# Performance work log

Hardware: AMD Instinct MI355X
Metric: run time of the kernel (lower is better)

Reference implementation:

```python
import jax, jax.numpy as jnp
import numpy as np

B, N, E, H = 2, 4096, 1024, 16
HD = E // H                      # head_dim = 64
R = 8                            # LoRA rank
LORA_SCALE = 16.0 / R            # alpha / r = 2.0
BUCKET_SIZES = (256, 64, 16)


def setup_inputs() -> dict:
    key = jax.random.key(0)
    ks = jax.random.split(key, 24)
    inp = {"x": jax.random.normal(ks[0], (B, N, E), jnp.float32)}
    inp["wb_coarse"] = jax.random.randint(ks[1], (B, N), 0, 16)
    inp["wb_mid"] = jax.random.randint(ks[2], (B, N), 0, 64)
    inp["wb_fine"] = jax.random.randint(ks[3], (B, N), 0, 256)
    i = 4
    for name in ("q", "k", "v", "o"):
        inp[f"W{name}"] = jax.random.normal(ks[i], (E, E), jnp.float32) / np.sqrt(E); i += 1
        inp[f"b{name}"] = jax.random.normal(ks[i], (E,), jnp.float32) * 0.01; i += 1
        inp[f"A{name}"] = jax.random.normal(ks[i], (R, E), jnp.float32) / np.sqrt(E); i += 1
        inp[f"B{name}"] = jax.random.normal(ks[i], (E, R), jnp.float32) * 0.01; i += 1
    return inp


def _lora(x, W, b, A, Bm):
    # F.linear(x, W, b) + scale * x @ A.T @ B.T   (dropout=0 in eval)
    return x @ W.T + b + LORA_SCALE * ((x @ A.T) @ Bm.T)


def _chunked_attn(q, k, v, bidx, C):
    # q,k,v: [BH, N, D]; bidx: [BH, N] int; C: chunk size (divides N)
    BH, Nn, D = q.shape
    sidx = jnp.argsort(bidx, axis=1)
    uidx = jnp.argsort(sidx, axis=1)
    g = lambda t, i: jnp.take_along_axis(t, i[..., None], axis=1)
    qs, ks_, vs = g(q, sidx), g(k, sidx), g(v, sidx)
    nc = Nn // C
    qs = qs.reshape(BH, nc, C, D)
    ks_ = ks_.reshape(BH, nc, C, D)
    vs = vs.reshape(BH, nc, C, D)
    # previous chunk (look-back of one chunk); chunk 0 has no previous -> masked
    k_prev = jnp.concatenate([jnp.zeros_like(ks_[:, :1]), ks_[:, :-1]], axis=1)
    v_prev = jnp.concatenate([jnp.zeros_like(vs[:, :1]), vs[:, :-1]], axis=1)
    k_cat = jnp.concatenate([k_prev, ks_], axis=2)   # [BH, nc, 2C, D]
    v_cat = jnp.concatenate([v_prev, vs], axis=2)
    scores = jnp.einsum('bncd,bnkd->bnck', qs, k_cat) / jnp.sqrt(jnp.asarray(D, qs.dtype))
    # mask look-back keys for chunk 0 (torch path attends only within chunk 0)
    chunk_ids = jnp.arange(nc)[:, None, None]        # [nc,1,1]
    key_pos = jnp.arange(2 * C)[None, None, :]       # [1,1,2C]
    neg = jnp.finfo(scores.dtype).min
    scores = jnp.where((chunk_ids == 0) & (key_pos < C), neg, scores)
    attn = jax.nn.softmax(scores, axis=-1)
    out = jnp.einsum('bnck,bnkd->bncd', attn, v_cat).reshape(BH, Nn, D)
    return jnp.take_along_axis(out, uidx[..., None], axis=1)


def reference(x, wb_coarse, wb_mid, wb_fine,
              Wq, bq, Aq, Bq, Wk, bk, Ak, Bk,
              Wv, bv, Av, Bv, Wo, bo, Ao, Bo):
    q = _lora(x, Wq, bq, Aq, Bq)
    k = _lora(x, Wk, bk, Ak, Bk)
    v = _lora(x, Wv, bv, Av, Bv)
    to_heads = lambda t: t.reshape(B, N, H, HD).transpose(0, 2, 1, 3).reshape(B * H, N, HD)
    qh, kh, vh = to_heads(q), to_heads(k), to_heads(v)
    expand = lambda w: jnp.broadcast_to(w[:, None, :], (B, H, N)).reshape(B * H, N)
    wbs = (expand(wb_coarse), expand(wb_mid), expand(wb_fine))
    outs = (_chunked_attn(qh, kh, vh, wbs[0], BUCKET_SIZES[0])
            + _chunked_attn(qh, kh, vh, wbs[1], BUCKET_SIZES[1])
            + _chunked_attn(qh, kh, vh, wbs[2], BUCKET_SIZES[2])) / 3.0
    outs = outs.reshape(B, H, N, HD).transpose(0, 2, 1, 3).reshape(B, N, E)
    return _lora(outs, Wo, bo, Ao, Bo)
```

## Files before the change

kernel.cpp:

```cpp
#include <hip/hip_runtime.h>
#include <cstdint>
#include <cstddef>

#define BDIM 2
#define NTOK 4096
#define EDIM 1024
#define HEADS 16
#define HDIM 64
#define MROWS (BDIM * NTOK)

typedef unsigned short u16;
typedef __attribute__((ext_vector_type(8))) short bf16x8;
typedef __attribute__((ext_vector_type(8))) unsigned short u16x8;
typedef __attribute__((ext_vector_type(4))) float f32x4;

#define MFMA(a, b, c) __builtin_amdgcn_mfma_f32_16x16x32_bf16(a, b, c, 0, 0, 0)
#define BAR() asm volatile("s_barrier" ::: "memory")
#define SETPRIO(p) __builtin_amdgcn_s_setprio(p)

__device__ inline void split2(float x, u16& h, u16& l) {
    union { float f; unsigned u; } a;
    a.f = x;
    unsigned uh = a.u + 0x7fff + ((a.u >> 16) & 1);
    h = (u16)(uh >> 16);
    union { unsigned u; float f; } hf; hf.u = (unsigned)h << 16;
    a.f = x - hf.f;
    unsigned ul = a.u + 0x7fff + ((a.u >> 16) & 1);
    l = (u16)(ul >> 16);
}

__device__ inline u16 bf16rne(float x) {
    union { float f; unsigned u; } a; a.f = x;
    unsigned r = a.u + 0x7fff + ((a.u >> 16) & 1);
    return (u16)(r >> 16);
}

#define GLL(gp, lp) __builtin_amdgcn_global_load_lds( \
    (const __attribute__((address_space(1))) unsigned*)(gp), \
    (__attribute__((address_space(3))) unsigned*)(lp), 16, 0, 0)

__global__ __launch_bounds__(256) void build_weff4_kernel(
    const float* __restrict__ W0, const float* __restrict__ A0, const float* __restrict__ B0,
    const float* __restrict__ W1, const float* __restrict__ A1, const float* __restrict__ B1,
    const float* __restrict__ W2, const float* __restrict__ A2, const float* __restrict__ B2,
    const float* __restrict__ W3, const float* __restrict__ A3, const float* __restrict__ B3,
    u16* __restrict__ dh0, u16* __restrict__ dl0,
    u16* __restrict__ dh1, u16* __restrict__ dl1,
    u16* __restrict__ dh2, u16* __restrict__ dl2,
    u16* __restrict__ dh3, u16* __restrict__ dl3)
{
    int s = blockIdx.y;
    const float* W = (s == 0) ? W0 : (s == 1) ? W1 : (s == 2) ? W2 : W3;
    const float* A = (s == 0) ? A0 : (s == 1) ? A1 : (s == 2) ? A2 : A3;
    const float* Bm = (s == 0) ? B0 : (s == 1) ? B1 : (s == 2) ? B2 : B3;
    u16* dh = (s == 0) ? dh0 : (s == 1) ? dh1 : (s == 2) ? dh2 : dh3;
    u16* dl = (s == 0) ? dl0 : (s == 1) ? dl1 : (s == 2) ? dl2 : dl3;

    int idx = blockIdx.x * 256 + threadIdx.x;
    int o = idx >> 10, i = idx & 1023;
    float sum = 0.f;
#pragma unroll
    for (int r = 0; r < 8; ++r) sum += Bm[o * 8 + r] * A[r * 1024 + i];
    float w = W[idx] + 2.0f * sum;
    u16 h, l;
    split2(w, h, l);
    dh[idx] = h; dl[idx] = l;
}

__global__ __launch_bounds__(256) void split_kernel(
    const float* __restrict__ src, u16* __restrict__ dh, u16* __restrict__ dl)
{
    int idx = blockIdx.x * 256 + threadIdx.x;
    float4 v = ((const float4*)src)[idx];
    ushort4 h, l;
    split2(v.x, h.x, l.x);
    split2(v.y, h.y, l.y);
    split2(v.z, h.z, l.z);
    split2(v.w, h.w, l.w);
    ((ushort4*)dh)[idx] = h;
    ((ushort4*)dl)[idx] = l;
}

__global__ __launch_bounds__(256) void sort3_kernel(
    const int* __restrict__ w0, const int* __restrict__ w1,
    const int* __restrict__ w2, int* __restrict__ sidx)
{
    __shared__ int sb[NTOK];
    __shared__ int cnt[32][256];
    __shared__ int gb[256];
    const int* srcs[3] = {w0, w1, w2};
    int t = threadIdx.x;
    const int* w = srcs[blockIdx.y] + blockIdx.x * NTOK;
    int* outp = sidx + ((int)blockIdx.y * BDIM + (int)blockIdx.x) * NTOK;

    for (int i = t; i < NTOK; i += 256) sb[i] = w[i];
    for (int i = t; i < 32 * 256; i += 256) ((int*)cnt)[i] = 0;
    __syncthreads();

    int g = t >> 3;
#pragma unroll
    for (int e = 0; e < 16; ++e)
        atomicAdd(&cnt[g][sb[g * 128 + (t & 7) + 8 * e]], 1);
    __syncthreads();

    int run = 0;
#pragma unroll
    for (int gg = 0; gg < 32; ++gg) {
        int c = cnt[gg][t];
        cnt[gg][t] = run;
        run += c;
    }
    gb[t] = run;
    __syncthreads();
    if (t == 0) {
        int acc = 0;
        for (int v = 0; v < 256; ++v) { int c = gb[v]; gb[v] = acc; acc += c; }
    }
    __syncthreads();
    for (int i = t; i < 32 * 256; i += 256) {
        int v = i & 255, gg = i >> 8;
        cnt[gg][v] += gb[v];
    }
    __syncthreads();

    if (t < 32) {
        int base = t * 128;
        for (int e = 0; e < 128; ++e) {
            int v = sb[base + e];
            int p = cnt[t][v]++;
            outp[p] = base + e;
        }
    }
}

__global__ __launch_bounds__(512, 2) void gemm_qk_kernel(
    const u16* __restrict__ Xh, const u16* __restrict__ Xl,
    const u16* __restrict__ Wh, const u16* __restrict__ Wl,
    const float* __restrict__ bq, const float* __restrict__ bk,
    u16* __restrict__ qh, u16* __restrict__ ql,
    u16* __restrict__ kh, u16* __restrict__ kl)
{
    __shared__ __align__(16) unsigned char smem[147456];
    u16* lds = (u16*)smem;
    const int PA_h = 0, PA_l = 8192, PB_h = 16384, PB_l = 20480;

    int t = threadIdx.x;
    int lane = t & 63, wave = t >> 6;
    int bid = blockIdx.x;
    int wg = (bid & 7) * 64 + (bid >> 3);
    int bx = wg & 15, by = wg >> 4;
    int m0 = by * 256, n0 = bx * 128;

    int lrow = lane & 15, lq = lane >> 4;
    size_t aoff = (size_t)(m0 + wave * 32 + lrow) * EDIM + lq * 8;
    size_t boff = (size_t)(n0 + wave * 16 + lrow) * EDIM + lq * 8;
    int slabA = wave * 2;
    int sA0 = (wave >> 1) * 4;
    int sB0 = (wave & 1) * 4;
    f32x4 acc[4][4] = {};

#pragma unroll
    for (int tt = 0; tt < 2; ++tt) {
        u16* sbuf = lds + tt * 24576;
        int kk = tt * 32;
        GLL(Xh + aoff + kk,             sbuf + PA_h + (slabA + 0) * 512);
        GLL(Xh + aoff + kk + 16 * EDIM, sbuf + PA_h + (slabA + 1) * 512);
        GLL(Xl + aoff + kk,             sbuf + PA_l + (slabA + 0) * 512);
        GLL(Xl + aoff + kk + 16 * EDIM, sbuf + PA_l + (slabA + 1) * 512);
        GLL(Wh + boff + kk, sbuf + PB_h + wave * 512);
        GLL(Wl + boff + kk, sbuf + PB_l + wave * 512);
    }
    asm volatile("s_waitcnt vmcnt(6)" ::: "memory");
    BAR();

    for (int t32 = 0; t32 < 32; ++t32) {
        u16* rb = lds + (t32 % 3) * 24576;
        u16* sbuf = lds + ((t32 + 2) % 3) * 24576;
        bool pf = (t32 + 2) < 32;
        int kn = (t32 + 2) * 32;
        bf16x8 bhf[4], blf[4];
#pragma unroll
        for (int p = 0; p < 4; ++p) {
            if (p == 0) {
#pragma unroll
                for (int j = 0; j < 4; ++j) {
                    bhf[j] = *(const bf16x8*)(rb + PB_h + (sB0 + j) * 512 + lane * 8);
                    blf[j] = *(const bf16x8*)(rb + PB_l + (sB0 + j) * 512 + lane * 8);
                }
            }
            bf16x8 aph = *(const bf16x8*)(rb + PA_h + (sA0 + p) * 512 + lane * 8);
            bf16x8 apl = *(const bf16x8*)(rb + PA_l + (sA0 + p) * 512 + lane * 8);
            if (pf) {
                if (p == 0) {
                    GLL(Xh + aoff + kn,             sbuf + PA_h + (slabA + 0) * 512);
                    GLL(Xh + aoff + kn + 16 * EDIM, sbuf + PA_h + (slabA + 1) * 512);
                } else if (p == 1) {
                    GLL(Xl + aoff + kn,             sbuf + PA_l + (slabA + 0) * 512);
                    GLL(Xl + aoff + kn + 16 * EDIM, sbuf + PA_l + (slabA + 1) * 512);
                } else if (p == 2) {
                    GLL(Wh + boff + kn, sbuf + PB_h + wave * 512);
                    GLL(Wl + boff + kn, sbuf + PB_l + wave * 512);
                }
            }
            BAR();
            SETPRIO(1);
#pragma unroll
            for (int j = 0; j < 4; ++j) {
                acc[p][j] = MFMA(aph, bhf[j], acc[p][j]);
                acc[p][j] = MFMA(aph, blf[j], acc[p][j]);
                acc[p][j] = MFMA(apl, bhf[j], acc[p][j]);
            }
            SETPRIO(0);
            if (p == 3) {
                if (pf) asm volatile("s_waitcnt vmcnt(6)" ::: "memory");
                else    asm volatile("s_waitcnt vmcnt(0)" ::: "memory");
            }
            BAR();
        }
    }

    int proj = n0 >> 10;
    const float* bias = proj ? bk : bq;
    u16* ohp = proj ? kh : qh;
    u16* olp = proj ? kl : ql;
    int wm = (wave >> 1) * 64, wn = (wave & 1) * 64;
    int q4 = lane >> 4, l16 = lane & 15;
    int cb = (n0 & 1023) + wn;
    float bj[4];
#pragma unroll
    for (int j = 0; j < 4; ++j) bj[j] = bias[cb + j * 16 + l16];
    float* repw = (float*)smem + wave * 2176;
    int r8 = lane >> 3, c8 = lane & 7;
#pragma unroll
    for (int gph = 0; gph < 2; ++gph) {
#pragma unroll
        for (int ii = 0; ii < 2; ++ii)
#pragma unroll
            for (int j = 0; j < 4; ++j)
#pragma unroll
                for (int r = 0; r < 4; ++r)
                    repw[(ii * 16 + q4 * 4 + r) * 68 + j * 16 + l16] =
                        acc[gph * 2 + ii][j][r] + bj[j];
#pragma unroll
        for (int rg = 0; rg < 4; ++rg) {
            int lr = rg * 8 + r8;
            float4 f0 = *(float4*)(repw + lr * 68 + c8 * 8);
            float4 f1 = *(float4*)(repw + lr * 68 + c8 * 8 + 4);
            float fa[8] = {f0.x, f0.y, f0.z, f0.w, f1.x, f1.y, f1.z, f1.w};
            size_t off = (size_t)(m0 + wm + gph * 32 + lr) * EDIM + cb + c8 * 8;
            u16x8 hv, lv;
#pragma unroll
            for (int e = 0; e < 8; ++e) {
                float v = fa[e];
                if (proj == 0) v *= 0.125f;
                u16 hh, ll;
                split2(v, hh, ll);
                hv[e] = hh; lv[e] = ll;
            }
            *(u16x8*)(ohp + off) = hv;
            *(u16x8*)(olp + off) = lv;
        }
    }
}

__global__ __launch_bounds__(512, 2) void gemm_v_kernel(
    const u16* __restrict__ Xh, const u16* __restrict__ Wv,
    const float* __restrict__ bv, u16* __restrict__ vh)
{
    __shared__ __align__(16) unsigned char smem[73728];
    u16* lds = (u16*)smem;

    int t = threadIdx.x;
    int lane = t & 63, wave = t >> 6;
    int bid = blockIdx.x;
    int wg = (bid & 7) * 32 + (bid >> 3);
    int bx = wg & 7, by = wg >> 3;
    int m0 = by * 256, nc0 = bx * 128;

    int lrow = lane & 15, lq = lane >> 4;
    size_t aoff = (size_t)(m0 + wave * 32 + lrow) * EDIM + lq * 8;
    size_t boff = (size_t)(nc0 + wave * 16 + lrow) * EDIM + lq * 8;
    int slabA = wave * 2;
    int sA0 = (wave >> 1) * 4;
    int sB0 = (wave & 1) * 4;
    f32x4 acc[4][4] = {};

#pragma unroll
    for (int tt = 0; tt < 2; ++tt) {
        u16* sbuf = lds + tt * 12288;
        int kk = tt * 32;
        GLL(Xh + aoff + kk,             sbuf + (slabA + 0) * 512);
        GLL(Xh + aoff + kk + 16 * EDIM, sbuf + (slabA + 1) * 512);
        GLL(Wv + boff + kk,             sbuf + 8192 + wave * 512);
    }
    asm volatile("s_waitcnt vmcnt(3)" ::: "memory");
    BAR();

    for (int t32 = 0; t32 < 32; ++t32) {
        u16* rb = lds + (t32 % 3) * 12288;
        u16* sbuf = lds + ((t32 + 2) % 3) * 12288;
        bool pf = (t32 + 2) < 32;
        int kn = (t32 + 2) * 32;

        bf16x8 bhf[4];
#pragma unroll
        for (int j = 0; j < 4; ++j)
            bhf[j] = *(const bf16x8*)(rb + 8192 + (sB0 + j) * 512 + lane * 8);
        bf16x8 a0 = *(const bf16x8*)(rb + (sA0 + 0) * 512 + lane * 8);
        bf16x8 a1 = *(const bf16x8*)(rb + (sA0 + 1) * 512 + lane * 8);
        if (pf) {
            GLL(Xh + aoff + kn,             sbuf + (slabA + 0) * 512);
            GLL(Xh + aoff + kn + 16 * EDIM, sbuf + (slabA + 1) * 512);
        }
        BAR();
        SETPRIO(1);
#pragma unroll
        for (int j = 0; j < 4; ++j) {
            acc[0][j] = MFMA(a0, bhf[j], acc[0][j]);
            acc[1][j] = MFMA(a1, bhf[j], acc[1][j]);
        }
        SETPRIO(0);
        BAR();

        bf16x8 a2 = *(const bf16x8*)(rb + (sA0 + 2) * 512 + lane * 8);
        bf16x8 a3 = *(const bf16x8*)(rb + (sA0 + 3) * 512 + lane * 8);
        if (pf) GLL(Wv + boff + kn, sbuf + 8192 + wave * 512);
        BAR();
        SETPRIO(1);
#pragma unroll
        for (int j = 0; j < 4; ++j) {
            acc[2][j] = MFMA(a2, bhf[j], acc[2][j]);
            acc[3][j] = MFMA(a3, bhf[j], acc[3][j]);
        }
        SETPRIO(0);
        if (pf) asm volatile("s_waitcnt vmcnt(3)" ::: "memory");
        else    asm volatile("s_waitcnt vmcnt(0)" ::: "memory");
        BAR();
    }

    int wm = (wave >> 1) * 64, wn = (wave & 1) * 64;
    int q4 = lane >> 4, l16 = lane & 15;
    int cb = nc0 + wn;
    float bj[4];
#pragma unroll
    for (int j = 0; j < 4; ++j) bj[j] = bv[cb + j * 16 + l16];
    float* repw = (float*)smem + wave * 2176;
    int r8 = lane >> 3, c8 = lane & 7;
#pragma unroll
    for (int gph = 0; gph < 2; ++gph) {
#pragma unroll
        for (int ii = 0; ii < 2; ++ii)
#pragma unroll
            for (int j = 0; j < 4; ++j)
#pragma unroll
                for (int r = 0; r < 4; ++r)
                    repw[(ii * 16 + q4 * 4 + r) * 68 + j * 16 + l16] =
                        acc[gph * 2 + ii][j][r] + bj[j];
#pragma unroll
        for (int rg = 0; rg < 4; ++rg) {
            int lr = rg * 8 + r8;
            float4 f0 = *(float4*)(repw + lr * 68 + c8 * 8);
            float4 f1 = *(float4*)(repw + lr * 68 + c8 * 8 + 4);
            float fa[8] = {f0.x, f0.y, f0.z, f0.w, f1.x, f1.y, f1.z, f1.w};
            size_t off = (size_t)(m0 + wm + gph * 32 + lr) * EDIM + cb + c8 * 8;
            u16x8 hv;
#pragma unroll
            for (int e = 0; e < 8; ++e) hv[e] = bf16rne(fa[e]);
            *(u16x8*)(vh + off) = hv;
        }
    }
}

__global__ __launch_bounds__(512, 2) void gemm_o_kernel(
    const u16* __restrict__ Xh, const u16* __restrict__ Xl,
    const u16* __restrict__ Wh, const u16* __restrict__ Wl,
    const float* __restrict__ bias, float* __restrict__ Y)
{
    __shared__ __align__(16) unsigned char smem[147456];
    u16* lds = (u16*)smem;
    const int PA_h = 0, PA_l = 8192, PB_h = 16384, PB_l = 20480;

    int t = threadIdx.x;
    int lane = t & 63, wave = t >> 6;
    int bid = blockIdx.x;
    int wg = (bid & 7) * 32 + (bid >> 3);
    int bx = wg & 7, by = wg >> 3;
    int m0 = by * 256, n0 = bx * 128;

    int lrow = lane & 15, lq = lane >> 4;
    size_t aoff = (size_t)(m0 + wave * 32 + lrow) * EDIM + lq * 8;
    size_t boff = (size_t)(n0 + wave * 16 + lrow) * EDIM + lq * 8;
    int slabA = wave * 2;
    int sA0 = (wave >> 1) * 4;
    int sB0 = (wave & 1) * 4;
    f32x4 acc[4][4] = {};

#pragma unroll
    for (int tt = 0; tt < 2; ++tt) {
        u16* sbuf = lds + tt * 24576;
        int kk = tt * 32;
        GLL(Xh + aoff + kk,             sbuf + PA_h + (slabA + 0) * 512);
        GLL(Xh + aoff + kk + 16 * EDIM, sbuf + PA_h + (slabA + 1) * 512);
        GLL(Xl + aoff + kk,             sbuf + PA_l + (slabA + 0) * 512);
        GLL(Xl + aoff + kk + 16 * EDIM, sbuf + PA_l + (slabA + 1) * 512);
        GLL(Wh + boff + kk, sbuf + PB_h + wave * 512);
        GLL(Wl + boff + kk, sbuf + PB_l + wave * 512);
    }
    asm volatile("s_waitcnt vmcnt(6)" ::: "memory");
    BAR();

    for (int t32 = 0; t32 < 32; ++t32) {
        u16* rb = lds + (t32 % 3) * 24576;
        u16* sbuf = lds + ((t32 + 2) % 3) * 24576;
        bool pf = (t32 + 2) < 32;
        int kn = (t32 + 2) * 32;
        bf16x8 bhf[4], blf[4];
#pragma unroll
        for (int p = 0; p < 4; ++p) {
            if (p == 0) {
#pragma unroll
                for (int j = 0; j < 4; ++j) {
                    bhf[j] = *(const bf16x8*)(rb + PB_h + (sB0 + j) * 512 + lane * 8);
                    blf[j] = *(const bf16x8*)(rb + PB_l + (sB0 + j) * 512 + lane * 8);
                }
            }
            bf16x8 aph = *(const bf16x8*)(rb + PA_h + (sA0 + p) * 512 + lane * 8);
            bf16x8 apl = *(const bf16x8*)(rb + PA_l + (sA0 + p) * 512 + lane * 8);
            if (pf) {
                if (p == 0) {
                    GLL(Xh + aoff + kn,             sbuf + PA_h + (slabA + 0) * 512);
                    GLL(Xh + aoff + kn + 16 * EDIM, sbuf + PA_h + (slabA + 1) * 512);
                } else if (p == 1) {
                    GLL(Xl + aoff + kn,             sbuf + PA_l + (slabA + 0) * 512);
                    GLL(Xl + aoff + kn + 16 * EDIM, sbuf + PA_l + (slabA + 1) * 512);
                } else if (p == 2) {
                    GLL(Wh + boff + kn, sbuf + PB_h + wave * 512);
                    GLL(Wl + boff + kn, sbuf + PB_l + wave * 512);
                }
            }
            BAR();
            SETPRIO(1);
#pragma unroll
            for (int j = 0; j < 4; ++j) {
                acc[p][j] = MFMA(aph, bhf[j], acc[p][j]);
                acc[p][j] = MFMA(aph, blf[j], acc[p][j]);
                acc[p][j] = MFMA(apl, bhf[j], acc[p][j]);
            }
            SETPRIO(0);
            if (p == 3) {
                if (pf) asm volatile("s_waitcnt vmcnt(6)" ::: "memory");
                else    asm volatile("s_waitcnt vmcnt(0)" ::: "memory");
            }
            BAR();
        }
    }

    int wm = (wave >> 1) * 64, wn = (wave & 1) * 64;
    int col_in = lane & 15, rquad = lane >> 4;
#pragma unroll
    for (int j = 0; j < 4; ++j) {
        int col = n0 + wn + j * 16 + col_in;
        float bvv = bias[col];
#pragma unroll
        for (int i = 0; i < 4; ++i) {
            int mbase = m0 + wm + i * 16 + rquad * 4;
#pragma unroll
            for (int r = 0; r < 4; ++r)
                Y[(size_t)(mbase + r) * EDIM + col] = acc[i][j][r] + bvv;
        }
    }
}

template <int C, bool ACC, bool OSPLIT>
__global__ __launch_bounds__(256, 3) void attn_mfma_kernel(
    const u16* __restrict__ Qh, const u16* __restrict__ Ql,
    const u16* __restrict__ Kh, const u16* __restrict__ Kl,
    const u16* __restrict__ Vh, const int* __restrict__ sidx,
    float* __restrict__ out, u16* __restrict__ osh, u16* __restrict__ osl)
{
    __shared__ u16 KfH[2][4096], KfL[2][4096];
    __shared__ u16 VL[64 * 72];
    __shared__ u16 PbH[4 * 16 * 56];

    int t = threadIdx.x;
    int lane = t & 63, wave = t >> 6;
    int quad = lane >> 4, l16 = lane & 15;
    int bh = blockIdx.y, b = bh >> 4, h = bh & 15;
    int p0 = blockIdx.x * 128;
    const int* sxb = sidx + b * NTOK;

    int ptile[2], ws_[2], we_[2];
    bf16x8 qhf[2][2], qlf[2][2];
#pragma unroll
    for (int tq = 0; tq < 2; ++tq) {
        ptile[tq] = p0 + wave * 32 + tq * 16;
        int c = ptile[tq] / C;
        ws_[tq] = (c > 0) ? (c - 1) * C : 0;
        we_[tq] = (c + 1) * C;
        int qrow = sxb[ptile[tq] + l16];
        size_t rb = (size_t)(b * NTOK + qrow) * EDIM + h * HDIM + quad * 8;
#pragma unroll
        for (int kk = 0; kk < 2; ++kk) {
            qhf[tq][kk] = *(const bf16x8*)(Qh + rb + kk * 32);
            qlf[tq][kk] = *(const bf16x8*)(Ql + rb + kk * 32);
        }
    }

    f32x4 oacc[2][4] = {};
    float lpart[2][4] = {};
    float mrun[2] = {-1e30f, -1e30f};

    int c0 = p0 / C, c1 = (p0 + 127) / C;
    int kmin = (c0 > 0) ? (c0 - 1) * C : 0;
    int kmax = (c1 + 1) * C;
    int nsteps = (kmax - kmin + 63) >> 6;

    {
        int tok = sxb[min(kmin + wave * 16 + l16, NTOK - 1)];
        size_t rb = (size_t)(b * NTOK + tok) * EDIM + h * HDIM + quad * 8;
        GLL(Kh + rb,      &KfH[0][(wave * 2 + 0) * 512]);
        GLL(Kh + rb + 32, &KfH[0][(wave * 2 + 1) * 512]);
        GLL(Kl + rb,      &KfL[0][(wave * 2 + 0) * 512]);
        GLL(Kl + rb + 32, &KfL[0][(wave * 2 + 1) * 512]);
        bf16x8 vreg[2];
#pragma unroll
        for (int it = 0; it < 2; ++it) {
            int c = it * 256 + t;
            int key = c & 63, dg = c >> 6;
            int tok2 = sxb[min(kmin + key, NTOK - 1)];
            vreg[it] = *(const bf16x8*)(Vh + (size_t)(b * NTOK + tok2) * EDIM + h * HDIM + dg * 8);
        }
#pragma unroll
        for (int it = 0; it < 2; ++it) {
            int c = it * 256 + t;
            int key = c & 63, dg = c >> 6;
#pragma unroll
            for (int e = 0; e < 8; ++e)
                VL[(dg * 8 + e) * 72 + key] = (u16)vreg[it][e];
        }
        asm volatile("s_waitcnt vmcnt(0)" ::: "memory");
        __syncthreads();
    }

    int pb = 0;
    for (int s = 0; s < nsteps; ++s) {
        int ks = kmin + s * 64;
        int nk = min(64, kmax - ks);
        bool pf = (s + 1) < nsteps;
        bf16x8 vreg[2];
        if (pf) {
            int ks2 = ks + 64;
            int tok = sxb[min(ks2 + wave * 16 + l16, NTOK - 1)];
            size_t rb = (size_t)(b * NTOK + tok) * EDIM + h * HDIM + quad * 8;
            GLL(Kh + rb,      &KfH[pb ^ 1][(wave * 2 + 0) * 512]);
            GLL(Kh + rb + 32, &KfH[pb ^ 1][(wave * 2 + 1) * 512]);
            GLL(Kl + rb,      &KfL[pb ^ 1][(wave * 2 + 0) * 512]);
            GLL(Kl + rb + 32, &KfL[pb ^ 1][(wave * 2 + 1) * 512]);
#pragma unroll
            for (int it = 0; it < 2; ++it) {
                int c = it * 256 + t;
                int key = c & 63, dg = c >> 6;
                int tok2 = sxb[min(ks2 + key, NTOK - 1)];
                vreg[it] = *(const bf16x8*)(Vh + (size_t)(b * NTOK + tok2) * EDIM + h * HDIM + dg * 8);
            }
        }

        int jlo0 = max(ks, ws_[0]) - ks, jhi0 = min(ks + nk, we_[0]) - ks;
        int jlo1 = max(ks, ws_[1]) - ks, jhi1 = min(ks + nk, we_[1]) - ks;
        bool e0 = jlo0 < jhi0, e1 = jlo1 < jhi1;
        if (e0 || e1) {
            int glo = e0 ? (e1 ? min(jlo0, jlo1) : jlo0) : jlo1;
            int ghi = e0 ? (e1 ? max(jhi0, jhi1) : jhi0) : jhi1;
            const u16* kfh = &KfH[pb][0];
            const u16* kfl = &KfL[pb][0];

            for (int g0 = glo & ~31; g0 < ghi; g0 += 32) {
                int s0i = g0 >> 4;
                int s1i = min(s0i + 1, 3);
                bf16x8 kh0[2], kl0[2], kh1[2], kl1[2];
#pragma unroll
                for (int kk = 0; kk < 2; ++kk) {
                    kh0[kk] = *(const bf16x8*)(kfh + ((s0i * 2 + kk) * 64 + lane) * 8);
                    kl0[kk] = *(const bf16x8*)(kfl + ((s0i * 2 + kk) * 64 + lane) * 8);
                    kh1[kk] = *(const bf16x8*)(kfh + ((s1i * 2 + kk) * 64 + lane) * 8);
                    kl1[kk] = *(const bf16x8*)(kfl + ((s1i * 2 + kk) * 64 + lane) * 8);
                }
#pragma unroll
                for (int tq = 0; tq < 2; ++tq) {
                    int jl = tq ? jlo1 : jlo0, jh = tq ? jhi1 : jhi0;
                    bool v0 = (g0 >= jl) && (g0 < jh);
                    bool v1 = (g0 + 16 >= jl) && (g0 + 16 < jh);
                    if (!v0 && !v1) continue;
                    f32x4 sa = {0.f, 0.f, 0.f, 0.f}, sb2 = {0.f, 0.f, 0.f, 0.f};
                    SETPRIO(1);
                    if (v0) {
                        sa = MFMA(qhf[tq][0], kh0[0], sa);
                        sa = MFMA(qhf[tq][0], kl0[0], sa);
                        sa = MFMA(qlf[tq][0], kh0[0], sa);
                        sa = MFMA(qhf[tq][1], kh0[1], sa);
                        sa = MFMA(qhf[tq][1], kl0[1], sa);
                        sa = MFMA(qlf[tq][1], kh0[1], sa);
                    }
                    if (v1) {
                        sb2 = MFMA(qhf[tq][0], kh1[0], sb2);
                        sb2 = MFMA(qhf[tq][0], kl1[0], sb2);
                        sb2 = MFMA(qlf[tq][0], kh1[0], sb2);
                        sb2 = MFMA(qhf[tq][1], kh1[1], sb2);
                        sb2 = MFMA(qhf[tq][1], kl1[1], sb2);
                        sb2 = MFMA(qlf[tq][1], kh1[1], sb2);
                    }
                    SETPRIO(0);
                    float smax = -1e30f;
                    if (v0) smax = fmaxf(smax, fmaxf(fmaxf(sa[0], sa[1]), fmaxf(sa[2], sa[3])));
                    if (v1) smax = fmaxf(smax, fmaxf(fmaxf(sb2[0], sb2[1]), fmaxf(sb2[2], sb2[3])));
                    smax = fmaxf(smax, __shfl_xor(smax, 1));
                    smax = fmaxf(smax, __shfl_xor(smax, 2));
                    smax = fmaxf(smax, __shfl_xor(smax, 4));
                    smax = fmaxf(smax, __shfl_xor(smax, 8));
                    float mold = mrun[tq];
                    float mnew = mold;
                    if (smax > mold + 8.0f) {
                        mnew = smax;
                        mrun[tq] = mnew;
                        float alpha = __expf(mold - mnew);
#pragma unroll
                        for (int r = 0; r < 4; ++r) lpart[tq][r] *= alpha;
#pragma unroll
                        for (int dt = 0; dt < 4; ++dt) {
                            oacc[tq][dt][0] *= alpha; oacc[tq][dt][1] *= alpha;
                            oacc[tq][dt][2] *= alpha; oacc[tq][dt][3] *= alpha;
                        }
                    }
                    u16* pbh = PbH + wave * 896;
#pragma unroll
                    for (int r = 0; r < 4; ++r) {
                        float pa = v0 ? __expf(sa[r] - mnew) : 0.f;
                        float pbv = v1 ? __expf(sb2[r] - mnew) : 0.f;
                        lpart[tq][r] += pa + pbv;
                        pbh[(quad * 4 + r) * 56 + l16] = bf16rne(pa);
                        pbh[(quad * 4 + r) * 56 + 16 + l16] = bf16rne(pbv);
                    }
                    bf16x8 ph = *(const bf16x8*)(pbh + l16 * 56 + quad * 8);
                    int kh2 = g0 >> 5;
                    SETPRIO(1);
#pragma unroll
                    for (int dt = 0; dt < 4; ++dt) {
                        bf16x8 vv = *(const bf16x8*)(VL + (dt * 16 + l16) * 72 + kh2 * 32 + quad * 8);
                        oacc[tq][dt] = MFMA(ph, vv, oacc[tq][dt]);
                    }
                    SETPRIO(0);
                }
            }
        }

        asm volatile("s_waitcnt vmcnt(0)" ::: "memory");
        __syncthreads();
        if (pf) {
#pragma unroll
            for (int it = 0; it < 2; ++it) {
                int c = it * 256 + t;
                int key = c & 63, dg = c >> 6;
#pragma unroll
                for (int e = 0; e < 8; ++e)
                    VL[(dg * 8 + e) * 72 + key] = (u16)vreg[it][e];
            }
        }
        __syncthreads();
        pb ^= 1;
    }

#pragma unroll
    for (int tq = 0; tq < 2; ++tq) {
        float inv[4];
#pragma unroll
        for (int r = 0; r < 4; ++r) {
            float v = lpart[tq][r];
            v += __shfl_xor(v, 1);
            v += __shfl_xor(v, 2);
            v += __shfl_xor(v, 4);
            v += __shfl_xor(v, 8);
            inv[r] = 1.0f / (3.0f * v);
        }
#pragma unroll
        for (int r = 0; r < 4; ++r) {
            int tok = sxb[ptile[tq] + quad * 4 + r];
            size_t base = (size_t)(b * NTOK + tok) * EDIM + h * HDIM + l16;
            if (OSPLIT) {
#pragma unroll
                for (int dt = 0; dt < 4; ++dt) {
                    float v = out[base + dt * 16] + oacc[tq][dt][r] * inv[r];
                    u16 hh, ll;
                    split2(v, hh, ll);
                    osh[base + dt * 16] = hh;
                    osl[base + dt * 16] = ll;
                }
            } else if (ACC) {
#pragma unroll
                for (int dt = 0; dt < 4; ++dt)
                    out[base + dt * 16] += oacc[tq][dt][r] * inv[r];
            } else {
#pragma unroll
                for (int dt = 0; dt < 4; ++dt)
                    out[base + dt * 16] = oacc[tq][dt][r] * inv[r];
            }
        }
    }
}

extern "C" void kernel_launch(void* const* d_in, const int* in_sizes, int n_in,
                              void* d_out, int out_size, void* d_ws, size_t ws_size,
                              hipStream_t stream)
{
    const float* x   = (const float*)d_in[0];
    const int*   wbc = (const int*)d_in[1];
    const int*   wbm = (const int*)d_in[2];
    const int*   wbf = (const int*)d_in[3];
    const float* Wq = (const float*)d_in[4],  *bq = (const float*)d_in[5];
    const float* Aq = (const float*)d_in[6],  *Bq = (const float*)d_in[7];
    const float* Wk = (const float*)d_in[8],  *bk = (const float*)d_in[9];
    const float* Ak = (const float*)d_in[10], *Bk = (const float*)d_in[11];
    const float* Wv = (const float*)d_in[12], *bv = (const float*)d_in[13];
    const float* Av = (const float*)d_in[14], *Bv = (const float*)d_in[15];
    const float* Wo = (const float*)d_in[16], *bo = (const float*)d_in[17];
    const float* Ao = (const float*)d_in[18], *Bo = (const float*)d_in[19];

    const size_t EE  = (size_t)EDIM * EDIM;
    const size_t BNE = (size_t)MROWS * EDIM;

    char* wsb = (char*)d_ws;
    float* ab = (float*)wsb;                        wsb += BNE * 4;
    u16* xh = (u16*)wsb;                            wsb += BNE * 2;
    u16* xl = (u16*)wsb;                            wsb += BNE * 2;
    u16* qh = (u16*)wsb;                            wsb += BNE * 2;
    u16* ql = (u16*)wsb;                            wsb += BNE * 2;
    u16* kh = (u16*)wsb;                            wsb += BNE * 2;
    u16* kl = (u16*)wsb;                            wsb += BNE * 2;
    u16* vh = (u16*)wsb;                            wsb += BNE * 2;
    u16* wh_all = (u16*)wsb;                        wsb += 3 * EE * 2;
    u16* wl_all = (u16*)wsb;                        wsb += 3 * EE * 2;
    u16* woh = (u16*)wsb;                           wsb += EE * 2;
    u16* wol = (u16*)wsb;                           wsb += EE * 2;
    int* sidx = (int*)wsb;                          wsb += 3 * BDIM * NTOK * 4;

    split_kernel<<<BNE / 1024, 256, 0, stream>>>(x, xh, xl);

    build_weff4_kernel<<<dim3(4096, 4), 256, 0, stream>>>(
        Wq, Aq, Bq, Wk, Ak, Bk, Wv, Av, Bv, Wo, Ao, Bo,
        wh_all + 0 * EE, wl_all + 0 * EE,
        wh_all + 1 * EE, wl_all + 1 * EE,
        wh_all + 2 * EE, wl_all + 2 * EE,
        woh, wol);

    sort3_kernel<<<dim3(BDIM, 3), 256, 0, stream>>>(wbc, wbm, wbf, sidx);

    gemm_qk_kernel<<<512, 512, 0, stream>>>(xh, xl, wh_all, wl_all,
                                            bq, bk, qh, ql, kh, kl);
    gemm_v_kernel<<<256, 512, 0, stream>>>(xh, wh_all + 2 * EE, bv, vh);

    dim3 ga(NTOK / 128, BDIM * HEADS);
    attn_mfma_kernel<256, false, false><<<ga, 256, 0, stream>>>(
        qh, ql, kh, kl, vh, sidx + 0 * BDIM * NTOK, ab, xh, xl);
    attn_mfma_kernel<64, true, false><<<ga, 256, 0, stream>>>(
        qh, ql, kh, kl, vh, sidx + 1 * BDIM * NTOK, ab, xh, xl);
    attn_mfma_kernel<16, true, true><<<ga, 256, 0, stream>>>(
        qh, ql, kh, kl, vh, sidx + 2 * BDIM * NTOK, ab, xh, xl);

    gemm_o_kernel<<<256, 512, 0, stream>>>(xh, xl, woh, wol, bo, (float*)d_out);
}
```

Measured before the change: 510.8 us.

## Merge three bucket attention passes into one launch with separate output buffers

```diff
diff --git a/kernel.cpp b/kernel.cpp
--- a/kernel.cpp
+++ b/kernel.cpp
@@ -81,6 +81,25 @@
     ((ushort4*)dl)[idx] = l;
 }
 
+__global__ __launch_bounds__(256) void sumsplit3_kernel(
+    const float* __restrict__ A, const float* __restrict__ B,
+    const float* __restrict__ Cc, u16* __restrict__ dh, u16* __restrict__ dl)
+{
+    int idx = blockIdx.x * 256 + threadIdx.x;
+    float4 a = ((const float4*)A)[idx];
+    float4 b = ((const float4*)B)[idx];
+    float4 c = ((const float4*)Cc)[idx];
+    float v[4] = {(a.x + b.x) + c.x, (a.y + b.y) + c.y,
+                  (a.z + b.z) + c.z, (a.w + b.w) + c.w};
+    ushort4 h, l;
+    split2(v[0], h.x, l.x);
+    split2(v[1], h.y, l.y);
+    split2(v[2], h.z, l.z);
+    split2(v[3], h.w, l.w);
+    ((ushort4*)dh)[idx] = h;
+    ((ushort4*)dl)[idx] = l;
+}
+
 __global__ __launch_bounds__(256) void sort3_kernel(
     const int* __restrict__ w0, const int* __restrict__ w1,
     const int* __restrict__ w2, int* __restrict__ sidx)
@@ -471,32 +490,38 @@
     }
 }
 
-template <int C, bool ACC, bool OSPLIT>
+template <int MODE>
 __global__ __launch_bounds__(256, 3) void attn_mfma_kernel(
     const u16* __restrict__ Qh, const u16* __restrict__ Ql,
     const u16* __restrict__ Kh, const u16* __restrict__ Kl,
-    const u16* __restrict__ Vh, const int* __restrict__ sidx,
-    float* __restrict__ out, u16* __restrict__ osh, u16* __restrict__ osl)
+    const u16* __restrict__ Vh, const int* __restrict__ sidx_base, int zofs,
+    float* __restrict__ out0, float* __restrict__ out1, float* __restrict__ out2,
+    u16* __restrict__ osh, u16* __restrict__ osl)
 {
     __shared__ u16 KfH[2][4096], KfL[2][4096];
     __shared__ u16 VL[64 * 72];
     __shared__ u16 PbH[4 * 16 * 56];
+
+    int sidx_i = blockIdx.z + zofs;
+    int lgC = 8 - 2 * sidx_i;
+    const int* sxb = sidx_base + sidx_i * BDIM * NTOK;
+    float* out = (sidx_i == 0) ? out0 : (sidx_i == 1) ? out1 : out2;
 
     int t = threadIdx.x;
     int lane = t & 63, wave = t >> 6;
     int quad = lane >> 4, l16 = lane & 15;
     int bh = blockIdx.y, b = bh >> 4, h = bh & 15;
     int p0 = blockIdx.x * 128;
-    const int* sxb = sidx + b * NTOK;
+    sxb += b * NTOK;
 
     int ptile[2], ws_[2], we_[2];
     bf16x8 qhf[2][2], qlf[2][2];
 #pragma unroll
     for (int tq = 0; tq < 2; ++tq) {
         ptile[tq] = p0 + wave * 32 + tq * 16;
-        int c = ptile[tq] / C;
-        ws_[tq] = (c > 0) ? (c - 1) * C : 0;
-        we_[tq] = (c + 1) * C;
+        int c = ptile[tq] >> lgC;
+        ws_[tq] = (c > 0) ? (c - 1) << lgC : 0;
+        we_[tq] = (c + 1) << lgC;
         int qrow = sxb[ptile[tq] + l16];
         size_t rb = (size_t)(b * NTOK + qrow) * EDIM + h * HDIM + quad * 8;
 #pragma unroll
@@ -510,9 +535,9 @@
     float lpart[2][4] = {};
     float mrun[2] = {-1e30f, -1e30f};
 
-    int c0 = p0 / C, c1 = (p0 + 127) / C;
-    int kmin = (c0 > 0) ? (c0 - 1) * C : 0;
-    int kmax = (c1 + 1) * C;
+    int c0 = p0 >> lgC, c1 = (p0 + 127) >> lgC;
+    int kmin = (c0 > 0) ? (c0 - 1) << lgC : 0;
+    int kmax = (c1 + 1) << lgC;
     int nsteps = (kmax - kmin + 63) >> 6;
 
     {
@@ -685,7 +710,7 @@
         for (int r = 0; r < 4; ++r) {
             int tok = sxb[ptile[tq] + quad * 4 + r];
             size_t base = (size_t)(b * NTOK + tok) * EDIM + h * HDIM + l16;
-            if (OSPLIT) {
+            if (MODE == 2) {
 #pragma unroll
                 for (int dt = 0; dt < 4; ++dt) {
                     float v = out[base + dt * 16] + oacc[tq][dt][r] * inv[r];
@@ -694,7 +719,7 @@
                     osh[base + dt * 16] = hh;
                     osl[base + dt * 16] = ll;
                 }
-            } else if (ACC) {
+            } else if (MODE == 1) {
 #pragma unroll
                 for (int dt = 0; dt < 4; ++dt)
                     out[base + dt * 16] += oacc[tq][dt][r] * inv[r];
@@ -741,6 +766,9 @@
     u16* woh = (u16*)wsb;                           wsb += EE * 2;
     u16* wol = (u16*)wsb;                           wsb += EE * 2;
     int* sidx = (int*)wsb;                          wsb += 3 * BDIM * NTOK * 4;
+    float* abC = (float*)wsb;
+    size_t need3 = (size_t)(wsb - (char*)d_ws) + BNE * 4;
+    bool merged = (ws_size >= need3);
 
     split_kernel<<<BNE / 1024, 256, 0, stream>>>(x, xh, xl);
 
@@ -757,13 +785,21 @@
                                             bq, bk, qh, ql, kh, kl);
     gemm_v_kernel<<<256, 512, 0, stream>>>(xh, wh_all + 2 * EE, bv, vh);
 
-    dim3 ga(NTOK / 128, BDIM * HEADS);
-    attn_mfma_kernel<256, false, false><<<ga, 256, 0, stream>>>(
-        qh, ql, kh, kl, vh, sidx + 0 * BDIM * NTOK, ab, xh, xl);
-    attn_mfma_kernel<64, true, false><<<ga, 256, 0, stream>>>(
-        qh, ql, kh, kl, vh, sidx + 1 * BDIM * NTOK, ab, xh, xl);
-    attn_mfma_kernel<16, true, true><<<ga, 256, 0, stream>>>(
-        qh, ql, kh, kl, vh, sidx + 2 * BDIM * NTOK, ab, xh, xl);
-
-    gemm_o_kernel<<<256, 512, 0, stream>>>(xh, xl, woh, wol, bo, (float*)d_out);
-}
+    if (merged) {
+        float* abB = (float*)xh;
+        dim3 ga3(NTOK / 128, BDIM * HEADS, 3);
+        attn_mfma_kernel<0><<<ga3, 256, 0, stream>>>(
+            qh, ql, kh, kl, vh, sidx, 0, ab, abB, abC, nullptr, nullptr);
+        sumsplit3_kernel<<<BNE / 1024, 256, 0, stream>>>(ab, abB, abC, qh, ql);
+        gemm_o_kernel<<<256, 512, 0, stream>>>(qh, ql, woh, wol, bo, (float*)d_out);
+    } else {
+        dim3 ga(NTOK / 128, BDIM * HEADS);
+        attn_mfma_kernel<0><<<ga, 256, 0, stream>>>(
+            qh, ql, kh, kl, vh, sidx, 0, ab, ab, ab, nullptr, nullptr);
+        attn_mfma_kernel<1><<<ga, 256, 0, stream>>>(
+            qh, ql, kh, kl, vh, sidx, 1, ab, ab, ab, nullptr, nullptr);
+        attn_mfma_kernel<2><<<ga, 256, 0, stream>>>(
+            qh, ql, kh, kl, vh, sidx, 2, ab, ab, ab, xh, xl);
+        gemm_o_kernel<<<256, 512, 0, stream>>>(xh, xl, woh, wol, bo, (float*)d_out);
+    }
+}
```

Measured after the change: 481.5 us. 5.7% less time.
